# Optimization experiments

Hardware: AMD Instinct MI355X
Metric: run time of the kernel (lower is better)

## Reference

```python
import jax, jax.numpy as jnp
import numpy as np
import math

B, T, C, H = 4, 1024, 1024, 16
D = C // H
EPS = 1e-5


def layer_norm(x, w, b):
    mu = jnp.mean(x, axis=-1, keepdims=True)
    var = jnp.mean(jnp.square(x - mu), axis=-1, keepdims=True)
    return (x - mu) * jax.lax.rsqrt(var + EPS) * w + b


def setup_inputs() -> dict:
    key = jax.random.key(0)
    ks = jax.random.split(key, 8)
    s = 0.02
    return {
        "x": jax.random.normal(ks[0], (B, T, C), jnp.float32),
        "attention_mask": jnp.ones((B, T), jnp.float32),
        "ln1_w": jnp.ones((C,), jnp.float32),
        "ln1_b": jnp.zeros((C,), jnp.float32),
        "w_attn": jax.random.normal(ks[1], (C, 3 * C), jnp.float32) * s,
        "b_attn": jnp.zeros((3 * C,), jnp.float32),
        "w_proj": jax.random.normal(ks[2], (C, C), jnp.float32) * s,
        "b_proj": jnp.zeros((C,), jnp.float32),
        "threshold": jnp.float32(0.0005),  # (layer_idx+1)/n_layer * final_token_threshold
        "ln2_w": jnp.ones((C,), jnp.float32),
        "ln2_b": jnp.zeros((C,), jnp.float32),
        "w_fc": jax.random.normal(ks[3], (C, 4 * C), jnp.float32) * s,
        "b_fc": jnp.zeros((4 * C,), jnp.float32),
        "w_fc2": jax.random.normal(ks[4], (4 * C, C), jnp.float32) * s,
        "b_fc2": jnp.zeros((C,), jnp.float32),
    }


def reference(x, attention_mask, ln1_w, ln1_b, w_attn, b_attn, w_proj, b_proj,
              threshold, ln2_w, ln2_b, w_fc, b_fc, w_fc2, b_fc2):
    # ---- attention (eval mode, dropout=0; hard masking_mode) ----
    h = layer_norm(x, ln1_w, ln1_b)
    qkv = h @ w_attn + b_attn                      # (B,T,3C)
    q, k, v = jnp.split(qkv, 3, axis=-1)
    q = q.reshape(B, T, H, D).transpose(0, 2, 1, 3)  # (B,H,T,D)
    k = k.reshape(B, T, H, D).transpose(0, 2, 1, 3)
    v = v.reshape(B, T, H, D).transpose(0, 2, 1, 3)

    scale = 1.0 / math.sqrt(D)
    logits = jnp.einsum("bhqd,bhkd->bhqk", q, k) * scale  # (B,H,T,T)
    causal = jnp.tril(jnp.ones((T, T), bool))
    neg_inf = jnp.float32(-jnp.inf)
    logits = jnp.where(causal[None, None], logits, neg_inf)
    # key-side validity mask (applied in original's manual pass; mask is all-ones
    # here so flash-path y == softmax(causal logits) @ v as well)
    logits = jnp.where(attention_mask[:, None, None, :] == 0, neg_inf, logits)
    att = jax.nn.softmax(logits, axis=-1)

    y = jnp.einsum("bhqk,bhkd->bhqd", att, v)      # (B,H,T,D)
    importance = att.mean(axis=1).mean(axis=1)     # (B,T): mean over heads, then queries

    y = y.transpose(0, 2, 1, 3).reshape(B, T, C)
    x = x + (y @ w_proj + b_proj)

    # ---- hard pruning mask ----
    pruning_mask = (importance >= threshold).astype(x.dtype)
    combined_mask = attention_mask * pruning_mask
    x = x * combined_mask[:, :, None]

    # ---- MLP ----
    h2 = layer_norm(x, ln2_w, ln2_b)
    f = jax.nn.gelu(h2 @ w_fc + b_fc, approximate=False)
    x = x + (f @ w_fc2 + b_fc2)

    pruning_loss = jnp.float32(0.0)  # hard mode -> always 0
    return (x, combined_mask, pruning_loss)
```

## Files before the change

kernel.cpp:

```cpp
#include <hip/hip_runtime.h>
#include <cstdint>
#include <cstring>

typedef unsigned short u16;
typedef short bf16x8 __attribute__((ext_vector_type(8)));
typedef float f32x4 __attribute__((ext_vector_type(4)));

#define MFMA16(a,b,c) __builtin_amdgcn_mfma_f32_16x16x32_bf16(a,b,c,0,0,0)


__device__ __forceinline__ u16 f2bf(float f) {
  union { float f; uint32_t u; } un; un.f = f;
  uint32_t u = un.u;
  u += 0x7FFFu + ((u >> 16) & 1u);
  return (u16)(u >> 16);
}

__device__ __forceinline__ float bf2f(u16 h) {
  union { uint32_t u; float f; } un; un.u = ((uint32_t)h) << 16;
  return un.f;
}

__device__ __forceinline__ float gelu_fast(float v) {
  float u = 0.7978845608028654f * (v + 0.044715f * v * v * v);
  float e = __expf(2.f * u);
  float th = 1.f - __fdividef(2.f, e + 1.f);
  return 0.5f * v * (1.f + th);
}

__device__ __forceinline__ void gl_lds16(const void* g, void* l) {
  __builtin_amdgcn_global_load_lds(
      (__attribute__((address_space(1))) void*)(const_cast<void*>(g)),
      (__attribute__((address_space(3))) void*)l, 16, 0, 0);
}


__global__ __launch_bounds__(256) void transpose_all(
    const float* __restrict__ wa, const float* __restrict__ wp,
    const float* __restrict__ wf, const float* __restrict__ wf2,
    u16* __restrict__ wat, u16* __restrict__ wpt,
    u16* __restrict__ wft, u16* __restrict__ wf2t)
{
  __shared__ float tile[32][33];
  int id = blockIdx.x;
  const float* W; u16* Wt; int K, N, bx, by;
  if (id < 3072)      { W = wa;  Wt = wat;  K = 1024; N = 3072; bx = id % 96;  by = id / 96; }
  else if (id < 4096) { id -= 3072; W = wp;  Wt = wpt;  K = 1024; N = 1024; bx = id % 32; by = id / 32; }
  else if (id < 8192) { id -= 4096; W = wf;  Wt = wft;  K = 1024; N = 4096; bx = id % 128; by = id / 128; }
  else                { id -= 8192; W = wf2; Wt = wf2t; K = 4096; N = 1024; bx = id % 32; by = id / 32; }
  int kt = by * 32, nt = bx * 32;
  int tx = threadIdx.x, ty = threadIdx.y;
#pragma unroll
  for (int i = 0; i < 4; ++i)
    tile[ty + i * 8][tx] = W[(size_t)(kt + ty + i * 8) * N + nt + tx];
  __syncthreads();
#pragma unroll
  for (int i = 0; i < 4; ++i)
    Wt[(size_t)(nt + ty + i * 8) * K + kt + tx] = f2bf(tile[tx][ty + i * 8]);
}


__global__ __launch_bounds__(256) void ln_bf16(
    const float* __restrict__ x, const float* __restrict__ wt,
    const float* __restrict__ bs, u16* __restrict__ out)
{
  int row = blockIdx.x;
  int tid = threadIdx.x, lane = tid & 63, w = tid >> 6;
  const float* xr = x + (size_t)row * 1024;
  float4 v = *(const float4*)(xr + tid * 4);
  float s = v.x + v.y + v.z + v.w;
  float sq = v.x * v.x + v.y * v.y + v.z * v.z + v.w * v.w;
#pragma unroll
  for (int o = 1; o < 64; o <<= 1) { s += __shfl_xor(s, o); sq += __shfl_xor(sq, o); }
  __shared__ float ls[4], lq[4];
  if (lane == 0) { ls[w] = s; lq[w] = sq; }
  __syncthreads();
  s = ls[0] + ls[1] + ls[2] + ls[3];
  sq = lq[0] + lq[1] + lq[2] + lq[3];
  float mu = s * (1.f / 1024.f);
  float var = sq * (1.f / 1024.f) - mu * mu;
  float rstd = rsqrtf(var + 1e-5f);
  float4 wv = *(const float4*)(wt + tid * 4);
  float4 bv = *(const float4*)(bs + tid * 4);
  ushort4 o4;
  o4.x = f2bf((v.x - mu) * rstd * wv.x + bv.x);
  o4.y = f2bf((v.y - mu) * rstd * wv.y + bv.y);
  o4.z = f2bf((v.z - mu) * rstd * wv.z + bv.z);
  o4.w = f2bf((v.w - mu) * rstd * wv.w + bv.w);
  *(ushort4*)(out + (size_t)row * 1024 + tid * 4) = o4;
}


__device__ __forceinline__ void gemm_mainloop_db(
    const u16* __restrict__ Abase, const u16* __restrict__ Bbase,
    int lda, int ldb, int nIter, f32x4 acc[4][4])
{
  __shared__ __align__(16) u16 lA[2][128 * 32];
  __shared__ __align__(16) u16 lB[2][128 * 32];

  const int tid = threadIdx.x;
  const int lane = tid & 63;
  const int w = tid >> 6;
  const int wr = (w >> 1) * 64;
  const int wc = (w & 1) * 64;
  const int laneM = lane & 15;
  const int laneK = (lane >> 4) * 8;

#pragma unroll
  for (int i = 0; i < 4; ++i)
#pragma unroll
    for (int j = 0; j < 4; ++j)
      acc[i][j] = f32x4{0.f, 0.f, 0.f, 0.f};

  const int off0 = w * 1024 + lane * 16;
  const int off1 = off0 + 4096;
  const int rA0 = off0 >> 6, cb0 = off0 & 63;
  const int rA1 = off1 >> 6, cb1 = off1 & 63;

  const size_t sA = (size_t)lda * 2;
  const size_t sB = (size_t)ldb * 2;
  const char* pA0 = (const char*)Abase + (size_t)rA0 * sA + cb0;
  const char* pA1 = (const char*)Abase + (size_t)rA1 * sA + cb1;
  const char* pB0 = (const char*)Bbase + (size_t)rA0 * sB + cb0;
  const char* pB1 = (const char*)Bbase + (size_t)rA1 * sB + cb1;
  char* dA0 = (char*)&lA[0][0] + off0;
  char* dA1 = (char*)&lA[0][0] + off1;
  char* dB0 = (char*)&lB[0][0] + off0;
  char* dB1 = (char*)&lB[0][0] + off1;

  gl_lds16(pA0, dA0); gl_lds16(pA1, dA1);
  gl_lds16(pB0, dB0); gl_lds16(pB1, dB1);
  pA0 += 64; pA1 += 64; pB0 += 64; pB1 += 64;
  __syncthreads();

  for (int it = 0; it < nIter; ++it) {
    const int cur = it & 1;
    const int nb = cur ^ 1;
    if (it + 1 < nIter) {
      gl_lds16(pA0, dA0 + nb * 8192);
      gl_lds16(pA1, dA1 + nb * 8192);
      gl_lds16(pB0, dB0 + nb * 8192);
      gl_lds16(pB1, dB1 + nb * 8192);
      pA0 += 64; pA1 += 64; pB0 += 64; pB1 += 64;
    }
    const u16* aRd = &lA[cur][(wr + laneM) * 32 + laneK];
    const u16* bRd = &lB[cur][(wc + laneM) * 32 + laneK];
    bf16x8 af[4], bfr[4];
#pragma unroll
    for (int t = 0; t < 4; ++t) {
      af[t]  = *(const bf16x8*)(aRd + t * 16 * 32);
      bfr[t] = *(const bf16x8*)(bRd + t * 16 * 32);
    }
#pragma unroll
    for (int i = 0; i < 4; ++i)
#pragma unroll
      for (int j = 0; j < 4; ++j)
        acc[i][j] = MFMA16(af[i], bfr[j], acc[i][j]);
    if (it + 1 < nIter) __syncthreads();
  }
}


__global__ __launch_bounds__(256, 4) void gemm_qkv(
    const u16* __restrict__ A, const u16* __restrict__ Bt,
    const float* __restrict__ bias,
    u16* __restrict__ qo, u16* __restrict__ ko, u16* __restrict__ vo)
{
  f32x4 acc[4][4];
  int m0 = blockIdx.y * 128, n0 = blockIdx.x * 128;
  gemm_mainloop_db(A + (size_t)m0 * 1024, Bt + (size_t)n0 * 1024, 1024, 1024, 32, acc);
  const int lane = threadIdx.x & 63, w = threadIdx.x >> 6;
  const int wr = (w >> 1) * 64, wc = (w & 1) * 64;
  const int laneM = lane & 15, q4 = lane >> 4;
  const int which = (n0 >> 10);
#pragma unroll
  for (int ti = 0; ti < 4; ++ti) {
#pragma unroll
    for (int tj = 0; tj < 4; ++tj) {
      int n = n0 + wc + tj * 16 + laneM;
      int c = n & 1023;
      int hh = c >> 6, d = c & 63;
      float bval = bias[n];
      if (which == 2) {
        int m0r = m0 + wr + ti * 16 + q4 * 4;
        int b = m0r >> 10, t0 = m0r & 1023;
        ushort4 o4;
        o4.x = f2bf(acc[ti][tj][0] + bval);
        o4.y = f2bf(acc[ti][tj][1] + bval);
        o4.z = f2bf(acc[ti][tj][2] + bval);
        o4.w = f2bf(acc[ti][tj][3] + bval);
        *(ushort4*)&vo[((size_t)((b * 16 + hh) * 64 + d)) * 1024 + t0] = o4;
      } else {
        u16* dst = (which == 0) ? qo : ko;
#pragma unroll
        for (int r = 0; r < 4; ++r) {
          int m = m0 + wr + ti * 16 + q4 * 4 + r;
          int b = m >> 10, t = m & 1023;
          dst[((size_t)((b * 16 + hh) * 1024 + t)) * 64 + d] = f2bf(acc[ti][tj][r] + bval);
        }
      }
    }
  }
}

__global__ __launch_bounds__(256, 4) void gemm_proj(
    const u16* __restrict__ A, const u16* __restrict__ Bt,
    const float* __restrict__ bias, const float* __restrict__ xin,
    const float* __restrict__ maskv, float* __restrict__ x2)
{
  f32x4 acc[4][4];
  int m0 = blockIdx.y * 128, n0 = blockIdx.x * 128;
  gemm_mainloop_db(A + (size_t)m0 * 1024, Bt + (size_t)n0 * 1024, 1024, 1024, 32, acc);
  const int lane = threadIdx.x & 63, w = threadIdx.x >> 6;
  const int wr = (w >> 1) * 64, wc = (w & 1) * 64;
  const int laneM = lane & 15, q4 = lane >> 4;
#pragma unroll
  for (int ti = 0; ti < 4; ++ti) {
#pragma unroll
    for (int tj = 0; tj < 4; ++tj) {
      int n = n0 + wc + tj * 16 + laneM;
      float bval = bias[n];
#pragma unroll
      for (int r = 0; r < 4; ++r) {
        int m = m0 + wr + ti * 16 + q4 * 4 + r;
        float v = xin[(size_t)m * 1024 + n] + acc[ti][tj][r] + bval;
        x2[(size_t)m * 1024 + n] = v * maskv[m];
      }
    }
  }
}

__global__ __launch_bounds__(256, 4) void gemm_fc(
    const u16* __restrict__ A, const u16* __restrict__ Bt,
    const float* __restrict__ bias, u16* __restrict__ fo)
{
  f32x4 acc[4][4];
  int m0 = blockIdx.y * 128, n0 = blockIdx.x * 128;
  gemm_mainloop_db(A + (size_t)m0 * 1024, Bt + (size_t)n0 * 1024, 1024, 1024, 32, acc);
  const int lane = threadIdx.x & 63, w = threadIdx.x >> 6;
  const int wr = (w >> 1) * 64, wc = (w & 1) * 64;
  const int laneM = lane & 15, q4 = lane >> 4;
#pragma unroll
  for (int ti = 0; ti < 4; ++ti) {
#pragma unroll
    for (int tj = 0; tj < 4; ++tj) {
      int n = n0 + wc + tj * 16 + laneM;
      float bval = bias[n];
#pragma unroll
      for (int r = 0; r < 4; ++r) {
        int m = m0 + wr + ti * 16 + q4 * 4 + r;
        fo[(size_t)m * 4096 + n] = f2bf(gelu_fast(acc[ti][tj][r] + bval));
      }
    }
  }
}

__global__ __launch_bounds__(256, 4) void gemm_fc2_splitk(
    const u16* __restrict__ A, const u16* __restrict__ Bt,
    u16* __restrict__ pall)
{
  int id = blockIdx.x;
  int r = id & 7, j = id >> 3;
  int mt = r * 4 + (j >> 5);
  int rem = j & 31;
  int n0 = (rem & 7) * 128;
  int kz = rem >> 3;
  int m0 = mt * 128;
  f32x4 acc[4][4];
  gemm_mainloop_db(A + (size_t)m0 * 4096 + kz * 1024,
                   Bt + (size_t)n0 * 4096 + kz * 1024, 4096, 4096, 32, acc);
  u16* p = pall + (size_t)kz * 4096 * 1024;
  const int lane = threadIdx.x & 63, w = threadIdx.x >> 6;
  const int wr = (w >> 1) * 64, wc = (w & 1) * 64;
  const int laneM = lane & 15, q4 = lane >> 4;
#pragma unroll
  for (int ti = 0; ti < 4; ++ti) {
#pragma unroll
    for (int tj = 0; tj < 4; ++tj) {
      int n = n0 + wc + tj * 16 + laneM;
#pragma unroll
      for (int r2 = 0; r2 < 4; ++r2) {
        int m = m0 + wr + ti * 16 + q4 * 4 + r2;
        p[(size_t)m * 1024 + n] = f2bf(acc[ti][tj][r2]);
      }
    }
  }
}

__global__ __launch_bounds__(256) void fc2_finalize(
    const float* __restrict__ x2, const float* __restrict__ bias,
    const u16* __restrict__ pall, float* __restrict__ out)
{
  int i = blockIdx.x * 256 + threadIdx.x;
  int col4 = i & 255;
  float4 a = ((const float4*)x2)[i];
  float4 b = ((const float4*)bias)[col4];
  float s0 = a.x + b.x, s1 = a.y + b.y, s2 = a.z + b.z, s3 = a.w + b.w;
#pragma unroll
  for (int z = 0; z < 4; ++z) {
    ushort4 u = ((const ushort4*)(pall + (size_t)z * 4194304))[i];
    s0 += bf2f(u.x); s1 += bf2f(u.y); s2 += bf2f(u.z); s3 += bf2f(u.w);
  }
  float4 o; o.x = s0; o.y = s1; o.z = s2; o.w = s3;
  ((float4*)out)[i] = o;
}


__global__ __launch_bounds__(256) void attn_fwd(
    const u16* __restrict__ qb, const u16* __restrict__ kb, const u16* __restrict__ vtb,
    u16* __restrict__ yb, float* __restrict__ part)
{
  const int bh = blockIdx.x;
  const int qbi = 7 - blockIdx.y;
  const int b = bh >> 4, h = bh & 15;
  const int tid = threadIdx.x, lane = tid & 63, w = tid >> 6;
  const int q0 = qbi * 128;
  const int laneM = lane & 15, q4 = lane >> 4;
  const float scale = 0.125f;

  __shared__ __align__(16) u16 lK[64 * 72];
  __shared__ __align__(16) u16 lV[64 * 72];
  __shared__ __align__(16) u16 lP[4][32 * 72];

  bf16x8 qf[2][2];
#pragma unroll
  for (int qs = 0; qs < 2; ++qs) {
    const u16* qrow = qb + ((size_t)(bh * 1024 + q0 + w * 32 + qs * 16 + laneM)) * 64 + q4 * 8;
    qf[qs][0] = *(const bf16x8*)qrow;
    qf[qs][1] = *(const bf16x8*)(qrow + 32);
  }

  const int nkt = 2 * qbi + 2;
  const int srow = tid >> 3;
  const int scol = (tid & 7) * 8;
  const u16* kbase = kb + (size_t)bh * 65536;
  const u16* vbase = vtb + (size_t)bh * 65536;

  float lrow[2][4] = {{0.f,0.f,0.f,0.f},{0.f,0.f,0.f,0.f}};
  for (int kt = 0; kt < nkt; ++kt) {
#pragma unroll
    for (int p = 0; p < 2; ++p) {
      int row = srow + p * 32;
      *(uint4*)&lK[row * 72 + scol] =
          *(const uint4*)(kbase + (size_t)(kt * 64 + row) * 64 + scol);
    }
    __syncthreads();
#pragma unroll
    for (int tj = 0; tj < 4; ++tj) {
      const u16* kp = &lK[(tj * 16 + laneM) * 72 + q4 * 8];
      bf16x8 k0 = *(const bf16x8*)kp;
      bf16x8 k1 = *(const bf16x8*)(kp + 32);
      int kc = kt * 64 + tj * 16 + laneM;
#pragma unroll
      for (int qs = 0; qs < 2; ++qs) {
        f32x4 z = {0.f, 0.f, 0.f, 0.f};
        z = MFMA16(qf[qs][0], k0, z);
        z = MFMA16(qf[qs][1], k1, z);
#pragma unroll
        for (int r = 0; r < 4; ++r) {
          int qg = q0 + w * 32 + qs * 16 + q4 * 4 + r;
          lrow[qs][r] += (kc <= qg) ? __expf(z[r] * scale) : 0.f;
        }
      }
    }
    __syncthreads();
  }
  float linv[2][4];
#pragma unroll
  for (int qs = 0; qs < 2; ++qs)
#pragma unroll
    for (int r = 0; r < 4; ++r) {
      float s = lrow[qs][r];
      s += __shfl_xor(s, 1); s += __shfl_xor(s, 2);
      s += __shfl_xor(s, 4); s += __shfl_xor(s, 8);
      linv[qs][r] = 1.f / s;
    }

  f32x4 o_[2][4];
#pragma unroll
  for (int qs = 0; qs < 2; ++qs)
#pragma unroll
    for (int dt = 0; dt < 4; ++dt) o_[qs][dt] = f32x4{0.f, 0.f, 0.f, 0.f};

  for (int kt = 0; kt < nkt; ++kt) {
#pragma unroll
    for (int p = 0; p < 2; ++p) {
      int row = srow + p * 32;
      *(uint4*)&lK[row * 72 + scol] =
          *(const uint4*)(kbase + (size_t)(kt * 64 + row) * 64 + scol);
      *(uint4*)&lV[row * 72 + scol] =
          *(const uint4*)(vbase + (size_t)row * 1024 + kt * 64 + scol);
    }
    __syncthreads();
    u16* lPw = &lP[w][0];
#pragma unroll
    for (int tj = 0; tj < 4; ++tj) {
      const u16* kp = &lK[(tj * 16 + laneM) * 72 + q4 * 8];
      bf16x8 k0 = *(const bf16x8*)kp;
      bf16x8 k1 = *(const bf16x8*)(kp + 32);
      int kc = kt * 64 + tj * 16 + laneM;
      float cs = 0.f;
#pragma unroll
      for (int qs = 0; qs < 2; ++qs) {
        f32x4 z = {0.f, 0.f, 0.f, 0.f};
        z = MFMA16(qf[qs][0], k0, z);
        z = MFMA16(qf[qs][1], k1, z);
#pragma unroll
        for (int r = 0; r < 4; ++r) {
          int qg = q0 + w * 32 + qs * 16 + q4 * 4 + r;
          float pv = (kc <= qg) ? __expf(z[r] * scale) * linv[qs][r] : 0.f;
          cs += pv;
          lPw[(qs * 16 + q4 * 4 + r) * 72 + tj * 16 + laneM] = f2bf(pv);
        }
      }
      cs += __shfl_xor(cs, 16);
      cs += __shfl_xor(cs, 32);
      if (lane < 16)
        atomicAdd(&part[(size_t)bh * 1024 + kt * 64 + tj * 16 + lane], cs);
    }
#pragma unroll
    for (int ss = 0; ss < 2; ++ss) {
#pragma unroll
      for (int qs = 0; qs < 2; ++qs) {
        bf16x8 pf = *(const bf16x8*)&lP[w][(qs * 16 + laneM) * 72 + ss * 32 + q4 * 8];
#pragma unroll
        for (int dt = 0; dt < 4; ++dt) {
          bf16x8 vf = *(const bf16x8*)&lV[(dt * 16 + laneM) * 72 + ss * 32 + q4 * 8];
          o_[qs][dt] = MFMA16(pf, vf, o_[qs][dt]);
        }
      }
    }
    __syncthreads();
  }

#pragma unroll
  for (int qs = 0; qs < 2; ++qs)
#pragma unroll
    for (int dt = 0; dt < 4; ++dt)
#pragma unroll
      for (int r = 0; r < 4; ++r) {
        int qg = q0 + w * 32 + qs * 16 + q4 * 4 + r;
        yb[((size_t)(b * 1024 + qg)) * 1024 + h * 64 + dt * 16 + laneM] = f2bf(o_[qs][dt][r]);
      }
}


__global__ __launch_bounds__(256) void finalize_mask(
    const float* __restrict__ part, const float* __restrict__ amask,
    const float* __restrict__ thr, float* __restrict__ mask_ws,
    float* __restrict__ out_mask, float* __restrict__ out_loss)
{
  int i = blockIdx.x * 256 + threadIdx.x;
  if (i >= 4096) return;
  int b = i >> 10;
  int t = i & 1023;
  float s = 0.f;
#pragma unroll
  for (int hh = 0; hh < 16; ++hh) s += part[(size_t)(b * 16 + hh) * 1024 + t];
  float imp = s * (1.0f / 16384.0f);
  float mv = (imp >= thr[0]) ? amask[i] : 0.f;
  mask_ws[i] = mv;
  out_mask[i] = mv;
  if (i == 0) out_loss[0] = 0.f;
}


extern "C" void kernel_launch(void* const* d_in, const int* in_sizes, int n_in,
                              void* d_out, int out_size, void* d_ws, size_t ws_size,
                              hipStream_t stream) {
  const float* x      = (const float*)d_in[0];
  const float* amask  = (const float*)d_in[1];
  const float* ln1w   = (const float*)d_in[2];
  const float* ln1b   = (const float*)d_in[3];
  const float* w_attn = (const float*)d_in[4];
  const float* b_attn = (const float*)d_in[5];
  const float* w_proj = (const float*)d_in[6];
  const float* b_proj = (const float*)d_in[7];
  const float* thr    = (const float*)d_in[8];
  const float* ln2w   = (const float*)d_in[9];
  const float* ln2b   = (const float*)d_in[10];
  const float* w_fc   = (const float*)d_in[11];
  const float* b_fc   = (const float*)d_in[12];
  const float* w_fc2  = (const float*)d_in[13];
  const float* b_fc2  = (const float*)d_in[14];
  float* out = (float*)d_out;

  char* ws = (char*)d_ws;
  size_t off = 0;
  auto alloc = [&](size_t bytes) -> char* {
    char* p = ws + off;
    off += (bytes + 255) & ~(size_t)255;
    return p;
  };
  u16* wattnT = (u16*)alloc((size_t)3072 * 1024 * 2);
  u16* wprojT = (u16*)alloc((size_t)1024 * 1024 * 2);
  u16* wfcT   = (u16*)alloc((size_t)4096 * 1024 * 2);
  u16* wfc2T  = (u16*)alloc((size_t)1024 * 4096 * 2);
  u16* hbuf   = (u16*)alloc((size_t)4096 * 1024 * 2);
  u16* qbuf   = (u16*)alloc((size_t)64 * 1024 * 64 * 2);
  u16* kbuf   = (u16*)alloc((size_t)64 * 1024 * 64 * 2);
  u16* vtbuf  = (u16*)alloc((size_t)64 * 64 * 1024 * 2);
  u16* ybuf   = (u16*)alloc((size_t)4096 * 1024 * 2);
  float* part = (float*)alloc((size_t)64 * 1024 * 4);
  float* maskws = (float*)alloc((size_t)4096 * 4);
  float* x2   = (float*)alloc((size_t)4096 * 1024 * 4);
  u16* h2     = (u16*)alloc((size_t)4096 * 1024 * 2);
  u16* fbuf   = (u16*)alloc((size_t)4096 * 4096 * 2);

  u16* pall = qbuf;

  transpose_all<<<12288, dim3(32, 8), 0, stream>>>(
      w_attn, w_proj, w_fc, w_fc2, wattnT, wprojT, wfcT, wfc2T);

  hipMemsetAsync(part, 0, (size_t)64 * 1024 * 4, stream);

  ln_bf16<<<4096, 256, 0, stream>>>(x, ln1w, ln1b, hbuf);

  gemm_qkv<<<dim3(24, 32), 256, 0, stream>>>(hbuf, wattnT, b_attn, qbuf, kbuf, vtbuf);

  attn_fwd<<<dim3(64, 8), 256, 0, stream>>>(qbuf, kbuf, vtbuf, ybuf, part);

  finalize_mask<<<16, 256, 0, stream>>>(part, amask, thr, maskws,
                                        out + 4194304, out + 4198400);

  gemm_proj<<<dim3(8, 32), 256, 0, stream>>>(ybuf, wprojT, b_proj, x, maskws, x2);

  ln_bf16<<<4096, 256, 0, stream>>>(x2, ln2w, ln2b, h2);

  gemm_fc<<<dim3(32, 32), 256, 0, stream>>>(h2, wfcT, b_fc, fbuf);

  gemm_fc2_splitk<<<1024, 256, 0, stream>>>(fbuf, wfc2T, pall);

  fc2_finalize<<<4096, 256, 0, stream>>>(x2, b_fc2, pall, out);
}
```

Before: 352.8 us.

## Pre-pack FC GEMM operands into MFMA fragment layout and load directly to registers

The LN2 output and the transposed w_fc weight are now written in a packed layout where each 16x32 MFMA fragment is contiguous. The fc GEMM then skips LDS staging and loads fragments straight from global memory into registers, double-buffering them across the K loop. This removes LDS traffic and barriers, but each wave now reads its own operands from global/L2 with no sharing inside the block, and launch bounds drop to 3 blocks per CU.

```diff
diff --git a/kernel.cpp b/kernel.cpp
--- a/kernel.cpp
+++ b/kernel.cpp
@@ -35,6 +35,7 @@
 }
 
 
+
 __global__ __launch_bounds__(256) void transpose_all(
     const float* __restrict__ wa, const float* __restrict__ wp,
     const float* __restrict__ wf, const float* __restrict__ wf2,
@@ -43,10 +44,10 @@
 {
   __shared__ float tile[32][33];
   int id = blockIdx.x;
-  const float* W; u16* Wt; int K, N, bx, by;
+  const float* W; u16* Wt; int K, N, bx, by; int packed = 0;
   if (id < 3072)      { W = wa;  Wt = wat;  K = 1024; N = 3072; bx = id % 96;  by = id / 96; }
   else if (id < 4096) { id -= 3072; W = wp;  Wt = wpt;  K = 1024; N = 1024; bx = id % 32; by = id / 32; }
-  else if (id < 8192) { id -= 4096; W = wf;  Wt = wft;  K = 1024; N = 4096; bx = id % 128; by = id / 128; }
+  else if (id < 8192) { id -= 4096; W = wf;  Wt = wft;  K = 1024; N = 4096; bx = id % 128; by = id / 128; packed = 1; }
   else                { id -= 8192; W = wf2; Wt = wf2t; K = 4096; N = 1024; bx = id % 32; by = id / 32; }
   int kt = by * 32, nt = bx * 32;
   int tx = threadIdx.x, ty = threadIdx.y;
@@ -54,9 +55,19 @@
   for (int i = 0; i < 4; ++i)
     tile[ty + i * 8][tx] = W[(size_t)(kt + ty + i * 8) * N + nt + tx];
   __syncthreads();
-#pragma unroll
-  for (int i = 0; i < 4; ++i)
-    Wt[(size_t)(nt + ty + i * 8) * K + kt + tx] = f2bf(tile[tx][ty + i * 8]);
+  if (!packed) {
+#pragma unroll
+    for (int i = 0; i < 4; ++i)
+      Wt[(size_t)(nt + ty + i * 8) * K + kt + tx] = f2bf(tile[tx][ty + i * 8]);
+  } else {
+#pragma unroll
+    for (int i = 0; i < 4; ++i) {
+      int n = nt + ty + i * 8, k = kt + tx;
+      size_t slot = ((size_t)(n >> 4) * 32 + (k >> 5)) * 512
+                  + (((k >> 3) & 3) * 16 + (n & 15)) * 8 + (k & 7);
+      Wt[slot] = f2bf(tile[tx][ty + i * 8]);
+    }
+  }
 }
 
 
@@ -91,6 +102,40 @@
 }
 
 
+__global__ __launch_bounds__(256) void ln_bf16_pack(
+    const float* __restrict__ x, const float* __restrict__ wt,
+    const float* __restrict__ bs, u16* __restrict__ out)
+{
+  int row = blockIdx.x;
+  int tid = threadIdx.x, lane = tid & 63, w = tid >> 6;
+  const float* xr = x + (size_t)row * 1024;
+  float4 v = *(const float4*)(xr + tid * 4);
+  float s = v.x + v.y + v.z + v.w;
+  float sq = v.x * v.x + v.y * v.y + v.z * v.z + v.w * v.w;
+#pragma unroll
+  for (int o = 1; o < 64; o <<= 1) { s += __shfl_xor(s, o); sq += __shfl_xor(sq, o); }
+  __shared__ float ls[4], lq[4];
+  if (lane == 0) { ls[w] = s; lq[w] = sq; }
+  __syncthreads();
+  s = ls[0] + ls[1] + ls[2] + ls[3];
+  sq = lq[0] + lq[1] + lq[2] + lq[3];
+  float mu = s * (1.f / 1024.f);
+  float var = sq * (1.f / 1024.f) - mu * mu;
+  float rstd = rsqrtf(var + 1e-5f);
+  float4 wv = *(const float4*)(wt + tid * 4);
+  float4 bv = *(const float4*)(bs + tid * 4);
+  ushort4 o4;
+  o4.x = f2bf((v.x - mu) * rstd * wv.x + bv.x);
+  o4.y = f2bf((v.y - mu) * rstd * wv.y + bv.y);
+  o4.z = f2bf((v.z - mu) * rstd * wv.z + bv.z);
+  o4.w = f2bf((v.w - mu) * rstd * wv.w + bv.w);
+  int c = tid * 4;
+  size_t slot = ((size_t)(row >> 4) * 32 + (c >> 5)) * 512
+              + (((c >> 3) & 3) * 16 + (row & 15)) * 8 + (c & 7);
+  *(ushort4*)(out + slot) = o4;
+}
+
+
 __device__ __forceinline__ void gemm_mainloop_db(
     const u16* __restrict__ Abase, const u16* __restrict__ Bbase,
     int lda, int ldb, int nIter, f32x4 acc[4][4])
@@ -230,25 +275,57 @@
   }
 }
 
-__global__ __launch_bounds__(256, 4) void gemm_fc(
-    const u16* __restrict__ A, const u16* __restrict__ Bt,
+__global__ __launch_bounds__(256, 3) void gemm_fc(
+    const u16* __restrict__ Ap, const u16* __restrict__ Bp,
     const float* __restrict__ bias, u16* __restrict__ fo)
 {
+  const int lane = threadIdx.x & 63, w = threadIdx.x >> 6;
+  const int m0 = blockIdx.y * 128 + (w >> 1) * 64;
+  const int n0 = blockIdx.x * 128 + (w & 1) * 64;
+  const int laneM = lane & 15, q4 = lane >> 4;
+
+  const u16* aBase = Ap + (size_t)(m0 >> 4) * 16384 + lane * 8;
+  const u16* bBase = Bp + (size_t)(n0 >> 4) * 16384 + lane * 8;
+
   f32x4 acc[4][4];
-  int m0 = blockIdx.y * 128, n0 = blockIdx.x * 128;
-  gemm_mainloop_db(A + (size_t)m0 * 1024, Bt + (size_t)n0 * 1024, 1024, 1024, 32, acc);
-  const int lane = threadIdx.x & 63, w = threadIdx.x >> 6;
-  const int wr = (w >> 1) * 64, wc = (w & 1) * 64;
-  const int laneM = lane & 15, q4 = lane >> 4;
+#pragma unroll
+  for (int i = 0; i < 4; ++i)
+#pragma unroll
+    for (int j = 0; j < 4; ++j)
+      acc[i][j] = f32x4{0.f, 0.f, 0.f, 0.f};
+
+  bf16x8 af[4], bfr[4], afn[4], bfn[4];
+#pragma unroll
+  for (int t = 0; t < 4; ++t) {
+    af[t]  = *(const bf16x8*)(aBase + (size_t)t * 16384);
+    bfr[t] = *(const bf16x8*)(bBase + (size_t)t * 16384);
+  }
+  for (int kb = 0; kb < 32; ++kb) {
+    if (kb + 1 < 32) {
+#pragma unroll
+      for (int t = 0; t < 4; ++t) {
+        afn[t] = *(const bf16x8*)(aBase + (size_t)t * 16384 + (kb + 1) * 512);
+        bfn[t] = *(const bf16x8*)(bBase + (size_t)t * 16384 + (kb + 1) * 512);
+      }
+    }
+#pragma unroll
+    for (int i = 0; i < 4; ++i)
+#pragma unroll
+      for (int j = 0; j < 4; ++j)
+        acc[i][j] = MFMA16(af[i], bfr[j], acc[i][j]);
+#pragma unroll
+    for (int t = 0; t < 4; ++t) { af[t] = afn[t]; bfr[t] = bfn[t]; }
+  }
+
 #pragma unroll
   for (int ti = 0; ti < 4; ++ti) {
 #pragma unroll
     for (int tj = 0; tj < 4; ++tj) {
-      int n = n0 + wc + tj * 16 + laneM;
+      int n = n0 + tj * 16 + laneM;
       float bval = bias[n];
 #pragma unroll
       for (int r = 0; r < 4; ++r) {
-        int m = m0 + wr + ti * 16 + q4 * 4 + r;
+        int m = m0 + ti * 16 + q4 * 4 + r;
         fo[(size_t)m * 4096 + n] = f2bf(gelu_fast(acc[ti][tj][r] + bval));
       }
     }
@@ -525,7 +602,7 @@
 
   gemm_proj<<<dim3(8, 32), 256, 0, stream>>>(ybuf, wprojT, b_proj, x, maskws, x2);
 
-  ln_bf16<<<4096, 256, 0, stream>>>(x2, ln2w, ln2b, h2);
+  ln_bf16_pack<<<4096, 256, 0, stream>>>(x2, ln2w, ln2b, h2);
 
   gemm_fc<<<dim3(32, 32), 256, 0, stream>>>(h2, wfcT, b_fc, fbuf);
 
```

Measured after the change: 353.4 us. No clear change (+0.2%).
